# Kernel tuning notes

Measured on AMD Instinct MI355X. Metric: run time of the kernel, lower is better.

The kernel has to match this reference:

```python
import jax, jax.numpy as jnp
import numpy as np

N, C, T, V = 32, 128, 128, 25
HS, HT, CI = 3, 2, 32
BN_INV = float(1.0 / np.sqrt(1.0 + 1e-5))  # eval-mode BN: running_mean=0, running_var=1


def conv1x1(x, w, b):
    # x: (N,C,T,V), w: (O,C), b: (O,)
    return jnp.einsum('nctv,oc->notv', x, w) + b[None, :, None, None]


def bn(x, g, b):
    return x * (g * BN_INV)[None, :, None, None] + b[None, :, None, None]


def lrelu(x):
    return jax.nn.leaky_relu(x, 0.1)


def setup_inputs() -> dict:
    key = jax.random.key(0)
    ks = jax.random.split(key, 16)
    w = lambda k, shp: jax.random.normal(k, shp, dtype=jnp.float32) * 0.05
    inp = {
        'x': jax.random.normal(ks[0], (N, C, T, V), dtype=jnp.float32),
        # spatial attention QK projection (conv 1x1): 2*HS*CI out channels
        'w_in_s': w(ks[1], (2 * HS * CI, C)), 'b_in_s': jnp.zeros((2 * HS * CI,), jnp.float32),
        'attention0s': jnp.ones((1, HS, V, V), jnp.float32) / V,
        'alphas': jnp.ones((1, HS, 1, 1), jnp.float32),
        'w_out_s': w(ks[2], (C, HS * C)), 'b_out_s': jnp.zeros((C,), jnp.float32),
        'g_out_s': jnp.ones((C,), jnp.float32), 'be_out_s': jnp.zeros((C,), jnp.float32),
        'w_ff_s': w(ks[3], (C, C)), 'b_ff_s': jnp.zeros((C,), jnp.float32),
        'g_ff_s': jnp.ones((C,), jnp.float32), 'be_ff_s': jnp.zeros((C,), jnp.float32),
        # temporal attention QK projection: 4*HT*CI out channels
        'w_in_t': w(ks[4], (4 * HT * CI, C)), 'b_in_t': jnp.zeros((4 * HT * CI,), jnp.float32),
        'alphat_f': jnp.ones((1, HT, 1, 1), jnp.float32),
        'alphat_b': jnp.ones((1, HT, 1, 1), jnp.float32),
        'w_out_t': w(ks[5], (C, 2 * HT * C)), 'b_out_t': jnp.zeros((C,), jnp.float32),
        'g_out_t': jnp.ones((C,), jnp.float32), 'be_out_t': jnp.zeros((C,), jnp.float32),
        'w_ff_t': w(ks[6], (C, C)), 'b_ff_t': jnp.zeros((C,), jnp.float32),
        'g_ff_t': jnp.ones((C,), jnp.float32), 'be_ff_t': jnp.zeros((C,), jnp.float32),
        # TCN: 7x1 temporal conv
        'w_tcn': w(ks[7], (C, C, 7, 1)), 'b_tcn': jnp.zeros((C,), jnp.float32),
        'g_tcn': jnp.ones((C,), jnp.float32), 'be_tcn': jnp.zeros((C,), jnp.float32),
    }
    return inp


def reference(x, w_in_s, b_in_s, attention0s, alphas, w_out_s, b_out_s, g_out_s, be_out_s,
              w_ff_s, b_ff_s, g_ff_s, be_ff_s, w_in_t, b_in_t, alphat_f, alphat_b,
              w_out_t, b_out_t, g_out_t, be_out_t, w_ff_t, b_ff_t, g_ff_t, be_ff_t,
              w_tcn, b_tcn, g_tcn, be_tcn):
    n = x.shape[0]
    # ---------------- spatial attention (S_atten='free', glo_reg_s) ----------------
    att_bias = attention0s[:, :, None]            # (1,HS,1,V,V) broadcast over T
    alphas_u = alphas[:, :, None]                 # (1,HS,1,1,1)
    qk = conv1x1(x, w_in_s, b_in_s).reshape(n, 2 * HS, CI, T, V)
    q, k = qk[:, :HS], qk[:, HS:]
    att = att_bias + jnp.tanh(jnp.einsum('nsctu,nsctv->nstuv', q, k) / CI) * alphas_u  # (N,HS,T,V,V)
    y = jnp.einsum('nctu,nstuv->nsctv', x, att).reshape(n, HS * C, T, V)
    y = bn(conv1x1(y, w_out_s, b_out_s), g_out_s, be_out_s)
    y = lrelu(x + y)                               # downs1 = identity (in==out, stride 1)
    y = bn(conv1x1(y, w_ff_s, b_ff_s), g_ff_s, be_ff_s)
    s_out = lrelu(x + y)                           # downs2 = identity
    # ---------------- temporal attention (directed, T_atten='context') ----------------
    z_in = s_out                                   # parallel=False -> temporal eats s_out
    qk_t = conv1x1(z_in, w_in_t, b_in_t).reshape(n, 4 * HT, CI, T, V)
    qt, kt = qk_t[:, :2 * HT], qk_t[:, 2 * HT:]
    qt = qt.mean(-1)                               # context attention: mean over joints -> (N,2HT,CI,T)
    kt = kt.mean(-1)
    att_t = jnp.tanh(jnp.einsum('nsct,nscu->nstu', qt, kt) / CI)  # (N,2HT,T,T)
    backward_mask = jnp.triu(jnp.ones((T, T), jnp.float32))
    forward_mask = backward_mask.T
    att_f = att_t[:, :HT] * alphat_f * forward_mask
    att_b = att_t[:, HT:] * alphat_b * backward_mask
    att_t = jnp.concatenate([att_f, att_b], axis=1)               # (N,2HT,T,T)
    z = jnp.einsum('nctv,nstu->nscuv', z_in, att_t).reshape(n, 2 * HT * C, T, V)
    z = bn(conv1x1(z, w_out_t, b_out_t), g_out_t, be_out_t)
    z = lrelu(z_in + z)                            # downt1 = identity
    z = bn(conv1x1(z, w_ff_t, b_ff_t), g_ff_t, be_ff_t)
    t_out = lrelu(z_in + z)                        # downt2 = identity
    # ---------------- TCN branch ----------------
    z2 = jax.lax.conv_general_dilated(t_out, w_tcn, (1, 1), ((3, 3), (0, 0)),
                                      dimension_numbers=('NCHW', 'OIHW', 'NCHW'))
    z2 = bn(z2 + b_tcn[None, :, None, None] * 0 + b_tcn[None, :, None, None], g_tcn, be_tcn) if False else bn(z2 + b_tcn[None, :, None, None], g_tcn, be_tcn)
    out = lrelu(t_out + z2)                        # downtTCN = identity
    return out
```

## Files before the change

### kernel.cpp

```cpp
#include <hip/hip_runtime.h>
#include <cstddef>

#define Nn 32
#define Cc 128
#define Tt 128
#define Vv 25
#define BN_INV 0.9999950000374997f


typedef __attribute__((ext_vector_type(8))) short bf16x8;
typedef __attribute__((ext_vector_type(4))) float f32x4;

__device__ __forceinline__ unsigned short f2bf(float f) {
    union { float f; unsigned u; } x; x.f = f;
    return (unsigned short)((x.u + 0x7FFFu + ((x.u >> 16) & 1u)) >> 16);
}
__device__ __forceinline__ float bf2f(unsigned short s) {
    union { unsigned u; float f; } x; x.u = ((unsigned)s) << 16;
    return x.f;
}


#define GFETCH(K0)                                                             \
    {                                                                          \
        int mg = m0 + sm;                                                      \
        if (mg < M) {                                                          \
            const unsigned short* ap = An + (size_t)mg*lda + (K0) + skh*16;    \
            a0n = *(const bf16x8*)ap;                                          \
            a1n = *(const bf16x8*)(ap + 8);                                    \
        }                                                                      \
        if (BMODE == 0) {                                                      \
            const unsigned short* Bn = (const unsigned short*)Bv               \
                                     + (size_t)n*bn_stride;                    \
            _Pragma("unroll")                                                  \
            for (int j = 0; j < 8; ++j)                                        \
                bqn[j] = Bn[(size_t)((K0) + skq*8 + j)*ldb + bcol];            \
        } else if (BMODE == 4) {                                               \
            const float* Bf = (const float*)Bv + (size_t)n*bn_stride;          \
            _Pragma("unroll")                                                  \
            for (int j = 0; j < 8; ++j)                                        \
                bqn[j] = f2bf(Bf[(size_t)((K0) + skq*8 + j)*ldb + bcol]);      \
        } else if (BMODE == 1) {                                               \
            const unsigned short* Bn = (const unsigned short*)Bv               \
                                     + (size_t)n*bn_stride;                    \
            int kb = (K0) + skq*8;                                             \
            int kidx = kb >> 7, c0 = kb & 127;                                 \
            int e = bcol + (kidx - 3)*25;                                      \
            bool ok = ((unsigned)e < 3200u);                                   \
            _Pragma("unroll")                                                  \
            for (int j = 0; j < 8; ++j)                                        \
                bqn[j] = ok ? Bn[(size_t)(c0 + j)*3200 + e] : (unsigned short)0;\
        } else {                                                  \
            const unsigned short* Bn = (const unsigned short*)Bv               \
                                     + (size_t)n*bn_stride;                    \
            int kb = (K0) + skq*8;                                             \
            int h = kb >> 7, t0b = kb & 127;                                   \
            const unsigned short* bp = Bn + (size_t)h*409600 + (size_t)bo*3200 \
                                          + (size_t)t0b*25 + bv_;              \
            _Pragma("unroll")                                                  \
            for (int j = 0; j < 8; ++j) bqn[j] = bp[j*25];                     \
        }                                                                      \
    }

template<int BMODE, int DMODE, int OM>
__global__ __launch_bounds__(256, 4) void gemm_k(
    const unsigned short* __restrict__ A, const void* __restrict__ Bv,
    float* __restrict__ D, unsigned short* __restrict__ Dbf,
    const float* __restrict__ resp, const float* __restrict__ bias,
    const float* __restrict__ gg, const float* __restrict__ bb,
    int M, int K, int lda, int ldb, int ldd,
    long an_stride, long bn_stride, long dn_stride, int gn, int gxn)
{
    __shared__ short Al[8*64*8];
    __shared__ short Bl[4*64*8];

    const int nwg = gridDim.x;
    const int b   = blockIdx.x;
    const int w   = (b & 7)*(nwg >> 3) + (b >> 3);
    const int n   = w / gxn;
    const int rem = w - n*gxn;
    const int mt  = rem / gn;
    const int nt  = rem - mt*gn;
    const int m0 = mt*128;
    const int j0 = nt*64;

    const unsigned short* An = A + (size_t)n*an_stride;

    const int tid = threadIdx.x;
    const int wav = tid >> 6, lane = tid & 63;
    const int lq = lane >> 4, l16 = lane & 15;

    const int sm  = tid >> 1, skh = tid & 1;
    const int scol = tid & 63, skq = tid >> 6;
    const int bcol = j0 + scol;

    int bo = 0, bv_ = 0;
    if (BMODE == 3) { bo = bcol/25; bv_ = bcol - 25*bo; }

    f32x4 acc[2][4];
    #pragma unroll
    for (int i = 0; i < 2; ++i)
        #pragma unroll
        for (int c = 0; c < 4; ++c) acc[i][c] = (f32x4){0.f,0.f,0.f,0.f};

    bf16x8 a0n = (bf16x8){0,0,0,0,0,0,0,0}, a1n = a0n;
    unsigned short bqn[8];
    GFETCH(0);

    for (int k0 = 0; k0 < K; k0 += 32) {
        __syncthreads();
        {
            short* Ap = Al + ((size_t)((sm>>4)*64 + (sm&15) + 32*skh))*8;
            *(bf16x8*)Ap = a0n;
            *(bf16x8*)(Ap + 128) = a1n;
        }
        {
            short* Bp = Bl + ((size_t)((scol>>4)*64 + skq*16 + (scol&15)))*8;
            bf16x8 p0;
            #pragma unroll
            for (int j = 0; j < 8; ++j) p0[j] = (short)bqn[j];
            *(bf16x8*)Bp = p0;
        }
        __syncthreads();

        if (k0 + 32 < K) GFETCH(k0 + 32);

        bf16x8 afr[2], bfr[4];
        afr[0] = *(const bf16x8*)(Al + ((size_t)((2*wav+0)*64 + lane))*8);
        afr[1] = *(const bf16x8*)(Al + ((size_t)((2*wav+1)*64 + lane))*8);
        #pragma unroll
        for (int c = 0; c < 4; ++c)
            bfr[c] = *(const bf16x8*)(Bl + ((size_t)(c*64 + lane))*8);
        #pragma unroll
        for (int i = 0; i < 2; ++i)
            #pragma unroll
            for (int c = 0; c < 4; ++c)
                acc[i][c] = __builtin_amdgcn_mfma_f32_16x16x32_bf16(
                    afr[i], bfr[c], acc[i][c], 0, 0, 0);
    }

    #pragma unroll
    for (int i = 0; i < 2; ++i) {
        const int mbase = m0 + (2*wav + i)*16 + lq*4;
        #pragma unroll
        for (int ct = 0; ct < 4; ++ct) {
            const int col = j0 + ct*16 + l16;
            if (DMODE == 0) {
                #pragma unroll
                for (int r = 0; r < 4; ++r) {
                    const int mg = mbase + r;
                    if (mg < M) {
                        const size_t addr = (size_t)mg*ldd + col + (size_t)n*dn_stride;
                        float val = acc[i][ct][r] + (bias ? bias[mg] : 0.f);
                        if (gg) {
                            val = val*(gg[mg]*BN_INV) + bb[mg] + resp[addr];
                            val = val > 0.f ? val : 0.1f*val;
                        }
                        if (OM != 1) D[addr] = val;
                        if (OM >= 1) Dbf[addr] = f2bf(val);
                    }
                }
            } else {
                const int c = col/25, v = col - 25*c;
                const float bi = bias ? bias[c] : 0.f;
                float gv = 0.f, b2 = 0.f;
                if (gg) { gv = gg[c]*BN_INV; b2 = bb[c]; }
                #pragma unroll
                for (int r = 0; r < 4; ++r) {
                    const int u = mbase + r;
                    const size_t addr = (size_t)c*3200 + (size_t)u*25 + v
                                      + (size_t)n*dn_stride;
                    float val = acc[i][ct][r] + bi;
                    if (gg) {
                        val = val*gv + b2 + resp[addr];
                        val = val > 0.f ? val : 0.1f*val;
                    }
                    if (OM != 1) D[addr] = val;
                    if (OM >= 1) Dbf[addr] = f2bf(val);
                }
            }
        }
    }
}

__global__ void k_prep(const float* __restrict__ wis, const float* __restrict__ wos,
                       const float* __restrict__ wfs, const float* __restrict__ wit,
                       const float* __restrict__ wot, const float* __restrict__ wft,
                       const float* __restrict__ wtc, unsigned short* __restrict__ W) {
    int i = blockIdx.x*256 + threadIdx.x;
    if (i < 24576) { W[i] = f2bf(wis[i]); return; }          i -= 24576;
    if (i < 49152) { W[24576 + i] = f2bf(wos[i]); return; }  i -= 49152;
    if (i < 16384) { W[73728 + i] = f2bf(wfs[i]); return; }  i -= 16384;
    if (i < 32768) { W[90112 + i] = f2bf(wit[i]); return; }  i -= 32768;
    if (i < 65536) {
        int ho = i >> 7, c = i & 127; int h = ho >> 7, o = ho & 127;
        W[122880 + i] = f2bf(wot[o*512 + h*128 + c]); return; } i -= 65536;
    if (i < 16384) { W[188416 + i] = f2bf(wft[i]); return; } i -= 16384;
    if (i < 114688) {
        int o = i / 896; int r = i - o*896; int kidx = r >> 7, c = r & 127;
        W[204800 + i] = f2bf(wtc[(o*128 + c)*7 + kidx]); }
}

__global__ void k_att_s(const unsigned short* __restrict__ qk,
                        const float* __restrict__ att0,
                        const float* __restrict__ alphas,
                        unsigned short* __restrict__ att) {
    int b = blockIdx.x;
    int n = b / (3*Tt); int rem = b - n*(3*Tt); int s = rem / Tt; int t = rem - s*Tt;
    __shared__ float qs[32*Vv], ks[32*Vv];
    const unsigned short* qp = qk + (size_t)n*614400 + (size_t)(s*32)*3200 + t*25;
    const unsigned short* kp = qk + (size_t)n*614400 + (size_t)(96 + s*32)*3200 + t*25;
    for (int i = threadIdx.x; i < 32*Vv; i += 256) {
        int c = i / Vv, v = i - c*Vv;
        qs[i] = bf2f(qp[(size_t)c*3200 + v]);
        ks[i] = bf2f(kp[(size_t)c*3200 + v]);
    }
    __syncthreads();
    float alpha = alphas[s];
    for (int i = threadIdx.x; i < Vv*Vv; i += 256) {
        int u = i / Vv, v = i - u*Vv;
        float a = 0.f;
        #pragma unroll
        for (int c = 0; c < 32; ++c) a += qs[c*Vv + u] * ks[c*Vv + v];
        att[(size_t)n*240000 + (size_t)s*80000 + (size_t)t*625 + i] =
            f2bf(att0[s*625 + i] + tanhf(a * (1.f/32.f)) * alpha);
    }
}

__global__ __launch_bounds__(256, 2) void k_eins_mfma(
    const float* __restrict__ X, const unsigned short* __restrict__ att,
    unsigned short* __restrict__ y2)
{
    __shared__ short Xf[128*128];
    __shared__ short Bf[7*4*64*8];

    const int n  = blockIdx.x >> 5;
    const int t0 = (blockIdx.x & 31) * 4;
    const int tid = threadIdx.x;
    const int wav = tid >> 6, lane = tid & 63;
    const int lq = lane >> 4, l16 = lane & 15;

    for (int i = tid; i < 7*4*64; i += 256)
        *(bf16x8*)(Bf + (size_t)i*8) = (bf16x8){0,0,0,0,0,0,0,0};

    const float* xp = X + (size_t)n*409600;
    for (int i = tid; i < 8192; i += 256) {
        int u2 = (i & 15)*2, tl = (i >> 4) & 3, c = i >> 6;
        float f0 = 0.f, f1 = 0.f;
        if (u2 < 25) {
            const float* p = xp + (size_t)c*3200 + (t0 + tl)*25 + u2;
            f0 = p[0];
            if (u2 < 24) f1 = p[1];
        }
        unsigned pk = (unsigned)f2bf(f0) | ((unsigned)f2bf(f1) << 16);
        int byte = (i*4) ^ ((c & 7) << 4);
        *(unsigned*)((char*)Xf + byte) = pk;
    }
    __syncthreads();

    bf16x8 afr[2][4];
    #pragma unroll
    for (int i = 0; i < 2; ++i) {
        const int c = (2*wav + i)*16 + l16;
        #pragma unroll
        for (int ks = 0; ks < 4; ++ks) {
            int byte = ((c*128 + ks*32 + lq*8)*2) ^ ((c & 7) << 4);
            afr[i][ks] = *(const bf16x8*)((const char*)Xf + byte);
        }
    }

    for (int s = 0; s < 3; ++s) {
        const unsigned short* ap = att + (size_t)n*240000 + (size_t)s*80000
                                       + (size_t)t0*625;
        for (int j = tid; j < 2500; j += 256) {
            int tl = j / 625, r = j - tl*625;
            int u = r / 25, v = r - u*25;
            int col = tl*25 + v;
            int l = ((u >> 3) << 4) | (col & 15);
            int nt = col >> 4;
            Bf[(size_t)((nt*4 + tl)*64 + l)*8 + (u & 7)] = (short)ap[j];
        }
        __syncthreads();

        f32x4 acc[2][7];
        #pragma unroll
        for (int i = 0; i < 2; ++i)
            #pragma unroll
            for (int nt = 0; nt < 7; ++nt) acc[i][nt] = (f32x4){0.f,0.f,0.f,0.f};

        #pragma unroll
        for (int ks = 0; ks < 4; ++ks) {
            bf16x8 bfr[7];
            #pragma unroll
            for (int nt = 0; nt < 7; ++nt)
                bfr[nt] = *(const bf16x8*)(Bf + (size_t)((nt*4 + ks)*64 + lane)*8);
            #pragma unroll
            for (int i = 0; i < 2; ++i)
                #pragma unroll
                for (int nt = 0; nt < 7; ++nt)
                    acc[i][nt] = __builtin_amdgcn_mfma_f32_16x16x32_bf16(
                        afr[i][ks], bfr[nt], acc[i][nt], 0, 0, 0);
        }

        unsigned short* yb = y2 + (size_t)n*1228800 + (size_t)(s*128)*3200 + t0*25;
        #pragma unroll
        for (int i = 0; i < 2; ++i) {
            const int row = (2*wav + i)*16 + lq*4;
            #pragma unroll
            for (int nt = 0; nt < 7; ++nt) {
                const int col = nt*16 + l16;
                if (col < 100) {
                    unsigned short* yp = yb + (size_t)row*3200 + col;
                    #pragma unroll
                    for (int r = 0; r < 4; ++r)
                        yp[(size_t)r*3200] = f2bf(acc[i][nt][r]);
                }
            }
        }
        __syncthreads();
    }
}

__global__ void k_mean(const float* __restrict__ X, unsigned short* __restrict__ xb) {
    int idx = blockIdx.x*256 + threadIdx.x;
    if (idx >= Nn*Cc*Tt) return;
    const float* p = X + (size_t)idx*25;
    float s = 0.f;
    #pragma unroll
    for (int v = 0; v < Vv; ++v) s += p[v];
    xb[idx] = f2bf(s * (1.f/25.f));
}

__global__ void k_att_t(const float* __restrict__ qkt, const float* __restrict__ af,
                        const float* __restrict__ ab, unsigned short* __restrict__ attb) {
    int n = blockIdx.x >> 2, h = blockIdx.x & 3;
    __shared__ float qs[32*Tt], ks[32*Tt];
    const float* qp = qkt + (size_t)n*32768 + (size_t)(h*32)*128;
    const float* kp = qkt + (size_t)n*32768 + (size_t)(128 + h*32)*128;
    for (int i = threadIdx.x; i < 32*Tt; i += 256) { qs[i] = qp[i]; ks[i] = kp[i]; }
    __syncthreads();
    float alpha = (h < 2) ? af[h] : ab[h-2];
    for (int i = threadIdx.x; i < Tt*Tt; i += 256) {
        int u = i >> 7, t = i & 127;
        bool keep = (h < 2) ? (t >= u) : (t <= u);
        float val = 0.f;
        if (keep) {
            float a = 0.f;
            #pragma unroll
            for (int c = 0; c < 32; ++c) a += qs[c*Tt + t] * ks[c*Tt + u];
            val = tanhf(a * (1.f/32.f)) * alpha;
        }
        attb[(size_t)n*65536 + (size_t)u*512 + h*128 + t] = f2bf(val);
    }
}

extern "C" void kernel_launch(void* const* d_in, const int* in_sizes, int n_in,
                              void* d_out, int out_size, void* d_ws, size_t ws_size,
                              hipStream_t stream) {
    const float* x       = (const float*)d_in[0];
    const float* w_in_s  = (const float*)d_in[1];
    const float* b_in_s  = (const float*)d_in[2];
    const float* att0s   = (const float*)d_in[3];
    const float* alphas  = (const float*)d_in[4];
    const float* w_out_s = (const float*)d_in[5];
    const float* b_out_s = (const float*)d_in[6];
    const float* g_out_s = (const float*)d_in[7];
    const float* be_out_s= (const float*)d_in[8];
    const float* w_ff_s  = (const float*)d_in[9];
    const float* b_ff_s  = (const float*)d_in[10];
    const float* g_ff_s  = (const float*)d_in[11];
    const float* be_ff_s = (const float*)d_in[12];
    const float* w_in_t  = (const float*)d_in[13];
    const float* b_in_t  = (const float*)d_in[14];
    const float* alphat_f= (const float*)d_in[15];
    const float* alphat_b= (const float*)d_in[16];
    const float* w_out_t = (const float*)d_in[17];
    const float* b_out_t = (const float*)d_in[18];
    const float* g_out_t = (const float*)d_in[19];
    const float* be_out_t= (const float*)d_in[20];
    const float* w_ff_t  = (const float*)d_in[21];
    const float* b_ff_t  = (const float*)d_in[22];
    const float* g_ff_t  = (const float*)d_in[23];
    const float* be_ff_t = (const float*)d_in[24];
    const float* w_tcn   = (const float*)d_in[25];
    const float* b_tcn   = (const float*)d_in[26];
    const float* g_tcn   = (const float*)d_in[27];
    const float* be_tcn  = (const float*)d_in[28];

    float* ws = (float*)d_ws;
    unsigned short* WB    = (unsigned short*)ws;
    unsigned short* QKBF  = (unsigned short*)(ws + 200000);
    unsigned short* S1BF  = (unsigned short*)(ws + 200000);
    unsigned short* ATSB  = (unsigned short*)(ws + 10030400);
    unsigned short* Y2BF  = (unsigned short*)(ws + 13870400);
    float*          SOUT  = ws + 33531200;
    unsigned short* ATTB  = (unsigned short*)(ws + 200000);
    unsigned short* XBARB = (unsigned short*)(ws + 1300000);
    float*          QKT   = ws + 1600000;
    unsigned short* TMPB  = (unsigned short*)(ws + 2700000);
    unsigned short* T1BF  = (unsigned short*)(ws + 46638400);
    float*          TOUT  = ws + 2700000;
    unsigned short* TOUTB = (unsigned short*)(ws + 15810000);
    float* out = (float*)d_out;

    unsigned short* wbis = WB;
    unsigned short* wbos = WB + 24576;
    unsigned short* wbfs = WB + 73728;
    unsigned short* wbit = WB + 90112;
    unsigned short* wbot = WB + 122880;
    unsigned short* wbft = WB + 188416;
    unsigned short* wbtc = WB + 204800;

    dim3 blk(256);
    const float* NUL = nullptr;

    k_prep<<<1248, blk, 0, stream>>>(w_in_s, w_out_s, w_ff_s, w_in_t,
                                     w_out_t, w_ff_t, w_tcn, WB);

    gemm_k<4,0,1><<<3200, blk, 0, stream>>>(
        wbis, x, nullptr, QKBF, NUL, b_in_s, NUL, NUL,
        192, 128, 128, 3200, 3200, 0L, 409600L, 614400L, 50, 100);
    k_att_s<<<Nn*3*Tt, blk, 0, stream>>>(QKBF, att0s, alphas, ATSB);
    k_eins_mfma<<<dim3(Nn*32), blk, 0, stream>>>(x, ATSB, Y2BF);
    gemm_k<0,0,1><<<1600, blk, 0, stream>>>(
        wbos, Y2BF, nullptr, S1BF, x, b_out_s, g_out_s, be_out_s,
        128, 384, 384, 3200, 3200, 0L, 1228800L, 409600L, 50, 50);
    gemm_k<0,0,0><<<1600, blk, 0, stream>>>(
        wbfs, S1BF, SOUT, nullptr, x, b_ff_s, g_ff_s, be_ff_s,
        128, 128, 128, 3200, 3200, 0L, 409600L, 409600L, 50, 50);

    k_mean<<<2048, blk, 0, stream>>>(SOUT, XBARB);
    gemm_k<0,0,0><<<128, blk, 0, stream>>>(
        wbit, XBARB, QKT, nullptr, NUL, b_in_t, NUL, NUL,
        256, 128, 128, 128, 128, 0L, 16384L, 32768L, 2, 4);
    k_att_t<<<Nn*4, blk, 0, stream>>>(QKT, alphat_f, alphat_b, ATTB);
    gemm_k<4,0,1><<<6400, blk, 0, stream>>>(
        wbot, SOUT, nullptr, TMPB, NUL, NUL, NUL, NUL,
        512, 128, 128, 3200, 3200, 0L, 409600L, 1638400L, 50, 200);
    gemm_k<3,2,1><<<1600, blk, 0, stream>>>(
        ATTB, TMPB, nullptr, T1BF, SOUT, b_out_t, g_out_t, be_out_t,
        128, 512, 512, 3200, 3200, 65536L, 1638400L, 409600L, 50, 50);
    gemm_k<0,0,2><<<1600, blk, 0, stream>>>(
        wbft, T1BF, TOUT, TOUTB, SOUT, b_ff_t, g_ff_t, be_ff_t,
        128, 128, 128, 3200, 3200, 0L, 409600L, 409600L, 50, 50);

    gemm_k<1,0,0><<<1600, blk, 0, stream>>>(
        wbtc, TOUTB, out, nullptr, TOUT, b_tcn, g_tcn, be_tcn,
        128, 896, 896, 3200, 3200, 0L, 409600L, 409600L, 50, 50);
}
```

Measured before the change: 710.0 us.

## Store bf16 GEMM operands position-major so B tiles load as 16-byte vectors

Several intermediate bf16 buffers (Y2, S1, XBAR, TOUT) change from channel-major to position-major (channel-contiguous) layout. Downstream GEMMs can then fetch B fragments with a single 16-byte vector load instead of eight strided scalar loads. A new epilogue mode transposes the output tile through shared memory so it can be written in the new layout. A zero-padded TOUT buffer, filled by a small k_zpad kernel, removes the bounds checks from the 7-tap temporal conv loads. The cost is extra LDS use and a sync in the transposing epilogue, plus one more kernel launch.

```diff
diff --git a/kernel.cpp b/kernel.cpp
--- a/kernel.cpp
+++ b/kernel.cpp
@@ -9,6 +9,7 @@
 
 
 typedef __attribute__((ext_vector_type(8))) short bf16x8;
+typedef __attribute__((ext_vector_type(4))) short short4v;
 typedef __attribute__((ext_vector_type(4))) float f32x4;
 
 __device__ __forceinline__ unsigned short f2bf(float f) {
@@ -50,7 +51,7 @@
             _Pragma("unroll")                                                  \
             for (int j = 0; j < 8; ++j)                                        \
                 bqn[j] = ok ? Bn[(size_t)(c0 + j)*3200 + e] : (unsigned short)0;\
-        } else {                                                  \
+        } else if (BMODE == 3) {                                               \
             const unsigned short* Bn = (const unsigned short*)Bv               \
                                      + (size_t)n*bn_stride;                    \
             int kb = (K0) + skq*8;                                             \
@@ -59,6 +60,18 @@
                                           + (size_t)t0b*25 + bv_;              \
             _Pragma("unroll")                                                  \
             for (int j = 0; j < 8; ++j) bqn[j] = bp[j*25];                     \
+        } else if (BMODE == 6) {                                               \
+            const unsigned short* Bn = (const unsigned short*)Bv               \
+                                     + (size_t)n*bn_stride;                    \
+            *(bf16x8*)bqn = *(const bf16x8*)(Bn + (size_t)bcol*ldb             \
+                                             + (K0) + skq*8);                  \
+        } else {                                                  \
+            const unsigned short* Bn = (const unsigned short*)Bv               \
+                                     + (size_t)n*bn_stride;                    \
+            int kb = (K0) + skq*8;                                             \
+            int kidx = kb >> 7, c0 = kb & 127;                                 \
+            long e = (long)bcol + (long)(kidx - 3)*25;                         \
+            *(bf16x8*)bqn = *(const bf16x8*)(Bn + e*128 + c0);                 \
         }                                                                      \
     }
 
@@ -69,10 +82,12 @@
     const float* __restrict__ resp, const float* __restrict__ bias,
     const float* __restrict__ gg, const float* __restrict__ bb,
     int M, int K, int lda, int ldb, int ldd,
-    long an_stride, long bn_stride, long dn_stride, int gn, int gxn)
+    long an_stride, long bn_stride, long dn_stride, long dbfn,
+    int gn, int gxn)
 {
     __shared__ short Al[8*64*8];
     __shared__ short Bl[4*64*8];
+    __shared__ __attribute__((aligned(16))) short Ot[(DMODE==1) ? 64*136 : 4];
 
     const int nwg = gridDim.x;
     const int b   = blockIdx.x;
@@ -104,7 +119,7 @@
         for (int c = 0; c < 4; ++c) acc[i][c] = (f32x4){0.f,0.f,0.f,0.f};
 
     bf16x8 a0n = (bf16x8){0,0,0,0,0,0,0,0}, a1n = a0n;
-    unsigned short bqn[8];
+    alignas(16) unsigned short bqn[8];
     GFETCH(0);
 
     for (int k0 = 0; k0 < K; k0 += 32) {
@@ -116,10 +131,7 @@
         }
         {
             short* Bp = Bl + ((size_t)((scol>>4)*64 + skq*16 + (scol&15)))*8;
-            bf16x8 p0;
-            #pragma unroll
-            for (int j = 0; j < 8; ++j) p0[j] = (short)bqn[j];
-            *(bf16x8*)Bp = p0;
+            *(bf16x8*)Bp = *(const bf16x8*)bqn;
         }
         __syncthreads();
 
@@ -139,44 +151,78 @@
                     afr[i], bfr[c], acc[i][c], 0, 0, 0);
     }
 
-    #pragma unroll
-    for (int i = 0; i < 2; ++i) {
-        const int mbase = m0 + (2*wav + i)*16 + lq*4;
-        #pragma unroll
-        for (int ct = 0; ct < 4; ++ct) {
-            const int col = j0 + ct*16 + l16;
-            if (DMODE == 0) {
+    if (DMODE == 1) {
+        #pragma unroll
+        for (int i = 0; i < 2; ++i) {
+            const int mbase = (2*wav + i)*16 + lq*4;
+            #pragma unroll
+            for (int ct = 0; ct < 4; ++ct) {
+                const int col = j0 + ct*16 + l16;
+                short4v pk;
                 #pragma unroll
                 for (int r = 0; r < 4; ++r) {
                     const int mg = mbase + r;
-                    if (mg < M) {
-                        const size_t addr = (size_t)mg*ldd + col + (size_t)n*dn_stride;
-                        float val = acc[i][ct][r] + (bias ? bias[mg] : 0.f);
+                    const size_t addr = (size_t)mg*ldd + col + (size_t)n*dn_stride;
+                    float val = acc[i][ct][r] + (bias ? bias[mg] : 0.f);
+                    if (gg) {
+                        val = val*(gg[mg]*BN_INV) + bb[mg] + resp[addr];
+                        val = val > 0.f ? val : 0.1f*val;
+                    }
+                    if (OM != 1) D[addr] = val;
+                    pk[r] = (short)f2bf(val);
+                }
+                *(short4v*)(Ot + (ct*16 + l16)*136 + mbase) = pk;
+            }
+        }
+        __syncthreads();
+        #pragma unroll
+        for (int j = 0; j < 4; ++j) {
+            int idx = j*256 + tid;
+            int cl = idx >> 4, m8 = (idx & 15)*8;
+            *(bf16x8*)(Dbf + (size_t)(j0 + cl)*128 + m8 + (size_t)n*dbfn)
+                = *(const bf16x8*)(Ot + cl*136 + m8);
+        }
+    } else {
+        #pragma unroll
+        for (int i = 0; i < 2; ++i) {
+            const int mbase = m0 + (2*wav + i)*16 + lq*4;
+            #pragma unroll
+            for (int ct = 0; ct < 4; ++ct) {
+                const int col = j0 + ct*16 + l16;
+                if (DMODE == 0) {
+                    #pragma unroll
+                    for (int r = 0; r < 4; ++r) {
+                        const int mg = mbase + r;
+                        if (mg < M) {
+                            const size_t addr = (size_t)mg*ldd + col
+                                              + (size_t)n*dn_stride;
+                            float val = acc[i][ct][r] + (bias ? bias[mg] : 0.f);
+                            if (gg) {
+                                val = val*(gg[mg]*BN_INV) + bb[mg] + resp[addr];
+                                val = val > 0.f ? val : 0.1f*val;
+                            }
+                            if (OM != 1) D[addr] = val;
+                            if (OM >= 1) Dbf[addr] = f2bf(val);
+                        }
+                    }
+                } else {
+                    const int c = col/25, v = col - 25*c;
+                    const float bi = bias ? bias[c] : 0.f;
+                    float gv = 0.f, b2 = 0.f;
+                    if (gg) { gv = gg[c]*BN_INV; b2 = bb[c]; }
+                    #pragma unroll
+                    for (int r = 0; r < 4; ++r) {
+                        const int u = mbase + r;
+                        const size_t addr = (size_t)c*3200 + (size_t)u*25 + v
+                                          + (size_t)n*dn_stride;
+                        float val = acc[i][ct][r] + bi;
                         if (gg) {
-                            val = val*(gg[mg]*BN_INV) + bb[mg] + resp[addr];
+                            val = val*gv + b2 + resp[addr];
                             val = val > 0.f ? val : 0.1f*val;
                         }
                         if (OM != 1) D[addr] = val;
                         if (OM >= 1) Dbf[addr] = f2bf(val);
                     }
-                }
-            } else {
-                const int c = col/25, v = col - 25*c;
-                const float bi = bias ? bias[c] : 0.f;
-                float gv = 0.f, b2 = 0.f;
-                if (gg) { gv = gg[c]*BN_INV; b2 = bb[c]; }
-                #pragma unroll
-                for (int r = 0; r < 4; ++r) {
-                    const int u = mbase + r;
-                    const size_t addr = (size_t)c*3200 + (size_t)u*25 + v
-                                      + (size_t)n*dn_stride;
-                    float val = acc[i][ct][r] + bi;
-                    if (gg) {
-                        val = val*gv + b2 + resp[addr];
-                        val = val > 0.f ? val : 0.1f*val;
-                    }
-                    if (OM != 1) D[addr] = val;
-                    if (OM >= 1) Dbf[addr] = f2bf(val);
                 }
             }
         }
@@ -201,6 +247,16 @@
         W[204800 + i] = f2bf(wtc[(o*128 + c)*7 + kidx]); }
 }
 
+__global__ void k_zpad(unsigned short* __restrict__ p) {
+    int i = blockIdx.x*256 + threadIdx.x;
+    if (i >= 76800) return;
+    int chunk = i*8;
+    int n = chunk / 19200;
+    int r = chunk - n*19200;
+    size_t addr = (size_t)n*428800 + (size_t)(r < 9600 ? r : 419200 + (r - 9600));
+    *(bf16x8*)(p + addr) = (bf16x8){0,0,0,0,0,0,0,0};
+}
+
 __global__ void k_att_s(const unsigned short* __restrict__ qk,
                         const float* __restrict__ att0,
                         const float* __restrict__ alphas,
@@ -302,7 +358,7 @@
                         afr[i][ks], bfr[nt], acc[i][nt], 0, 0, 0);
         }
 
-        unsigned short* yb = y2 + (size_t)n*1228800 + (size_t)(s*128)*3200 + t0*25;
+        unsigned short* yb = y2 + (size_t)n*1228800;
         #pragma unroll
         for (int i = 0; i < 2; ++i) {
             const int row = (2*wav + i)*16 + lq*4;
@@ -310,10 +366,10 @@
             for (int nt = 0; nt < 7; ++nt) {
                 const int col = nt*16 + l16;
                 if (col < 100) {
-                    unsigned short* yp = yb + (size_t)row*3200 + col;
+                    short4v pk;
                     #pragma unroll
-                    for (int r = 0; r < 4; ++r)
-                        yp[(size_t)r*3200] = f2bf(acc[i][nt][r]);
+                    for (int r = 0; r < 4; ++r) pk[r] = (short)f2bf(acc[i][nt][r]);
+                    *(short4v*)(yb + (size_t)(t0*25 + col)*384 + s*128 + row) = pk;
                 }
             }
         }
@@ -328,7 +384,8 @@
     float s = 0.f;
     #pragma unroll
     for (int v = 0; v < Vv; ++v) s += p[v];
-    xb[idx] = f2bf(s * (1.f/25.f));
+    int n = idx >> 14, rem = idx & 16383, c = rem >> 7, t = rem & 127;
+    xb[(size_t)n*16384 + (size_t)t*128 + c] = f2bf(s * (1.f/25.f));
 }
 
 __global__ void k_att_t(const float* __restrict__ qkt, const float* __restrict__ af,
@@ -393,6 +450,8 @@
     unsigned short* S1BF  = (unsigned short*)(ws + 200000);
     unsigned short* ATSB  = (unsigned short*)(ws + 10030400);
     unsigned short* Y2BF  = (unsigned short*)(ws + 13870400);
+    unsigned short* TOUTBP= (unsigned short*)(ws + 23710000);
+    unsigned short* TOUTB = TOUTBP + 9600;
     float*          SOUT  = ws + 33531200;
     unsigned short* ATTB  = (unsigned short*)(ws + 200000);
     unsigned short* XBARB = (unsigned short*)(ws + 1300000);
@@ -400,7 +459,6 @@
     unsigned short* TMPB  = (unsigned short*)(ws + 2700000);
     unsigned short* T1BF  = (unsigned short*)(ws + 46638400);
     float*          TOUT  = ws + 2700000;
-    unsigned short* TOUTB = (unsigned short*)(ws + 15810000);
     float* out = (float*)d_out;
 
     unsigned short* wbis = WB;
@@ -419,32 +477,33 @@
 
     gemm_k<4,0,1><<<3200, blk, 0, stream>>>(
         wbis, x, nullptr, QKBF, NUL, b_in_s, NUL, NUL,
-        192, 128, 128, 3200, 3200, 0L, 409600L, 614400L, 50, 100);
+        192, 128, 128, 3200, 3200, 0L, 409600L, 614400L, 614400L, 50, 100);
     k_att_s<<<Nn*3*Tt, blk, 0, stream>>>(QKBF, att0s, alphas, ATSB);
     k_eins_mfma<<<dim3(Nn*32), blk, 0, stream>>>(x, ATSB, Y2BF);
-    gemm_k<0,0,1><<<1600, blk, 0, stream>>>(
+    gemm_k<6,1,1><<<1600, blk, 0, stream>>>(
         wbos, Y2BF, nullptr, S1BF, x, b_out_s, g_out_s, be_out_s,
-        128, 384, 384, 3200, 3200, 0L, 1228800L, 409600L, 50, 50);
-    gemm_k<0,0,0><<<1600, blk, 0, stream>>>(
+        128, 384, 384, 384, 3200, 0L, 1228800L, 409600L, 409600L, 50, 50);
+    gemm_k<6,0,0><<<1600, blk, 0, stream>>>(
         wbfs, S1BF, SOUT, nullptr, x, b_ff_s, g_ff_s, be_ff_s,
-        128, 128, 128, 3200, 3200, 0L, 409600L, 409600L, 50, 50);
+        128, 128, 128, 128, 3200, 0L, 409600L, 409600L, 409600L, 50, 50);
 
     k_mean<<<2048, blk, 0, stream>>>(SOUT, XBARB);
-    gemm_k<0,0,0><<<128, blk, 0, stream>>>(
+    gemm_k<6,0,0><<<128, blk, 0, stream>>>(
         wbit, XBARB, QKT, nullptr, NUL, b_in_t, NUL, NUL,
-        256, 128, 128, 128, 128, 0L, 16384L, 32768L, 2, 4);
+        256, 128, 128, 128, 128, 0L, 16384L, 32768L, 32768L, 2, 4);
     k_att_t<<<Nn*4, blk, 0, stream>>>(QKT, alphat_f, alphat_b, ATTB);
     gemm_k<4,0,1><<<6400, blk, 0, stream>>>(
         wbot, SOUT, nullptr, TMPB, NUL, NUL, NUL, NUL,
-        512, 128, 128, 3200, 3200, 0L, 409600L, 1638400L, 50, 200);
+        512, 128, 128, 3200, 3200, 0L, 409600L, 1638400L, 1638400L, 50, 200);
     gemm_k<3,2,1><<<1600, blk, 0, stream>>>(
         ATTB, TMPB, nullptr, T1BF, SOUT, b_out_t, g_out_t, be_out_t,
-        128, 512, 512, 3200, 3200, 65536L, 1638400L, 409600L, 50, 50);
-    gemm_k<0,0,2><<<1600, blk, 0, stream>>>(
+        128, 512, 512, 3200, 3200, 65536L, 1638400L, 409600L, 409600L, 50, 50);
+    k_zpad<<<300, blk, 0, stream>>>(TOUTBP);
+    gemm_k<0,1,2><<<1600, blk, 0, stream>>>(
         wbft, T1BF, TOUT, TOUTB, SOUT, b_ff_t, g_ff_t, be_ff_t,
-        128, 128, 128, 3200, 3200, 0L, 409600L, 409600L, 50, 50);
-
-    gemm_k<1,0,0><<<1600, blk, 0, stream>>>(
+        128, 128, 128, 3200, 3200, 0L, 409600L, 409600L, 428800L, 50, 50);
+
+    gemm_k<7,0,0><<<1600, blk, 0, stream>>>(
         wbtc, TOUTB, out, nullptr, TOUT, b_tcn, g_tcn, be_tcn,
-        128, 896, 896, 3200, 3200, 0L, 409600L, 409600L, 50, 50);
-}
+        128, 896, 896, 0, 3200, 0L, 428800L, 409600L, 409600L, 50, 50);
+}
```

Result: no change. 706.3 us (-0.5%).
